# Performance work log

Measured on AMD Instinct MI355X. Metric: run time of the kernel, lower is better.

## Reference

```python
import jax, jax.numpy as jnp
import numpy as np

T, B = 32, 64
H, W = 16, 16
FEAT = 32
CNN_DIM = 512
N_ACT = 5
MAP_OUT = FEAT * H * W  # 8192, flattened map readout


def _conv_relu(x, w, b, stride):
    y = jax.lax.conv_general_dilated(
        x, w, (stride, stride), 'VALID',
        dimension_numbers=('NCHW', 'OIHW', 'NCHW'))
    return jax.nn.relu(y + b[None, :, None, None])


def _mlp(x, w1, b1, w2, b2):
    return jax.nn.relu(x @ w1 + b1) @ w2 + b2


def setup_inputs() -> dict:
    key = jax.random.key(0)
    ks = jax.random.split(key, 32)
    g = lambda k, shape, fan: jax.random.normal(k, shape, jnp.float32) * (1.0 / np.sqrt(fan))
    inp = {}
    inp['image'] = jax.random.uniform(ks[0], (T * B, 84, 84, 3), jnp.float32) * 255.0
    inp['done'] = jnp.zeros((T, B), jnp.float32)
    inp['state0'] = jnp.zeros((B, FEAT, H, W), jnp.float32)
    inp['position'] = jax.random.randint(ks[1], (T * B, 2), 0, H).astype(jnp.int32)
    # NatureCNN params
    inp['w1'] = g(ks[2], (32, 3, 8, 8), 3 * 8 * 8); inp['b1'] = jnp.zeros((32,), jnp.float32)
    inp['w2'] = g(ks[3], (64, 32, 4, 4), 32 * 4 * 4); inp['b2'] = jnp.zeros((64,), jnp.float32)
    inp['w3'] = g(ks[4], (64, 64, 3, 3), 64 * 3 * 3); inp['b3'] = jnp.zeros((64,), jnp.float32)
    inp['wfc'] = g(ks[5], (64 * 7 * 7, CNN_DIM), 64 * 7 * 7); inp['bfc'] = jnp.zeros((CNN_DIM,), jnp.float32)
    # Map write projection
    inp['Ww'] = g(ks[6], (CNN_DIM, FEAT), CNN_DIM); inp['bw'] = jnp.zeros((FEAT,), jnp.float32)
    # pos_net MLP: one-hot(16)+one-hot(16)=32 -> 64
    inp['wp1'] = g(ks[7], (2 * H, 64), 2 * H); inp['bp1'] = jnp.zeros((64,), jnp.float32)
    inp['wp2'] = g(ks[8], (64, 64), 64); inp['bp2'] = jnp.zeros((64,), jnp.float32)
    # policy MLP: (MAP_OUT+64) -> 64 -> N_ACT
    inp['wpo1'] = g(ks[9], (MAP_OUT + 64, 64), MAP_OUT + 64); inp['bpo1'] = jnp.zeros((64,), jnp.float32)
    inp['wpo2'] = g(ks[10], (64, N_ACT), 64) * 0.01; inp['bpo2'] = jnp.zeros((N_ACT,), jnp.float32)
    # value MLP
    inp['wv1'] = g(ks[11], (MAP_OUT + 64, 64), MAP_OUT + 64); inp['bv1'] = jnp.zeros((64,), jnp.float32)
    inp['wv2'] = g(ks[12], (64, 1), 64); inp['bv2'] = jnp.zeros((1,), jnp.float32)
    return inp


def reference(image, done, state0, w1, b1, w2, b2, w3, b3, wfc, bfc, Ww, bw,
              wp1, bp1, wp2, bp2, wpo1, bpo1, wpo2, bpo2, wv1, bv1, wv2, bv2,
              position):
    # preprocess_image: /255 and NHWC -> NCHW
    x = jnp.transpose(image / 255.0, (0, 3, 1, 2))
    x = _conv_relu(x, w1, b1, 4)   # [TB,32,20,20]
    x = _conv_relu(x, w2, b2, 2)   # [TB,64,9,9]
    x = _conv_relu(x, w3, b3, 1)   # [TB,64,7,7]
    h = jax.nn.relu(x.reshape(x.shape[0], -1) @ wfc + bfc)  # [TB,512]

    h_seq = h.reshape(T, B, CNN_DIM)
    idx_seq = position.reshape(T, B, 2)
    benv = jnp.arange(B)

    def step(state, inp):
        h_t, d_t, i_t = inp
        masked = (1.0 - d_t)[:, None, None, None] * state  # reset done envs
        wfeat = h_t @ Ww + bw                              # [B,FEAT]
        state = masked.at[benv, :, i_t[:, 0], i_t[:, 1]].add(wfeat)
        return state, state.reshape(B, -1)                 # per-step map readout

    state, outs = jax.lax.scan(step, state0, (h_seq, done, idx_seq))
    hidden = outs.reshape(T * B, MAP_OUT)

    # position net on one-hot coords
    pos_oh = jnp.concatenate([jax.nn.one_hot(position[:, 0], H, dtype=hidden.dtype),
                              jax.nn.one_hot(position[:, 1], W, dtype=hidden.dtype)], axis=1)
    pos_feat = _mlp(pos_oh, wp1, bp1, wp2, bp2)            # [TB,64]
    hidden = jnp.concatenate([hidden, pos_feat], axis=1)

    logits = _mlp(hidden, wpo1, bpo1, wpo2, bpo2)          # [TB,N_ACT]
    v = _mlp(hidden, wv1, bv1, wv2, bv2)                   # [TB,1]
    return logits, v, state
```

## Files before the change

### kernel.cpp

```cpp
#include <hip/hip_runtime.h>
#include <hip/hip_bf16.h>


#define TT 32
#define BB 64
#define TBR 2048

typedef _Float16 half_t;
typedef __attribute__((ext_vector_type(4))) _Float16 half4;
typedef __attribute__((ext_vector_type(8))) _Float16 half8;
typedef __attribute__((ext_vector_type(4))) float f32x4;

#define OFF_W1T   0u
#define OFF_W2T   6144u
#define OFF_W3T   22528u
#define OFF_WF    40960u
#define OFF_PF    106496u
#define OFF_Y0    237568u
#define OFF_YS    245760u
#define OFF_H     507904u
#define OFF_WFCT  1556480u
#define OFF_C3    2359296u
#define OFF_C2    5570560u
#define OFF_C1    10878976u

__global__ __launch_bounds__(256) void prep_kernel(
    const float* __restrict__ w1, const float* __restrict__ w2,
    const float* __restrict__ w3, half_t* __restrict__ w1p,
    half_t* __restrict__ w2T, half_t* __restrict__ w3T) {
  int g = blockIdx.x * 256 + threadIdx.x;
  if (g < 8192) {
    int kk = g & 31, oc = (g >> 5) & 31, tap = g >> 10;
    half_t v = (half_t)0.f;
    if (kk < 24) {
      int kx = kk / 3, c = kk - 3 * kx;
      v = (half_t)(w1[oc * 192 + c * 64 + tap * 8 + kx] * (1.0f / 255.0f));
    }
    w1p[g] = v;
    return;
  }
  int g2 = g - 8192;
  if (g2 < 32768) {
    int c = g2 & 31, oc = (g2 >> 5) & 63, tap = g2 >> 11;
    w2T[g2] = (half_t)w2[oc * 512 + c * 16 + tap];
    return;
  }
  int g3 = g2 - 32768;
  if (g3 < 36864) {
    int c = g3 & 63, oc = (g3 >> 6) & 63, tap = g3 >> 12;
    w3T[g3] = (half_t)w3[oc * 576 + c * 9 + tap];
  }
}

__global__ __launch_bounds__(256) void prep_wfct(
    const float* __restrict__ wfc, half_t* __restrict__ wfcT) {
  __shared__ float t[32][33];
  int k0 = blockIdx.x * 32, n0 = blockIdx.y * 32;
  int tx = threadIdx.x & 31, ty = threadIdx.x >> 5;
#pragma unroll
  for (int i = 0; i < 4; ++i)
    t[ty + 8 * i][tx] = wfc[(size_t)(k0 + ty + 8 * i) * 512 + n0 + tx];
  __syncthreads();
#pragma unroll
  for (int i = 0; i < 4; ++i)
    wfcT[(size_t)(n0 + ty + 8 * i) * 3136 + k0 + tx] =
        (half_t)t[tx][ty + 8 * i];
}

#define C1_BANDF 5040
#define C1_BANDV 1260
__global__ __launch_bounds__(256) void conv1_mfma(
    const float* __restrict__ img, const half_t* __restrict__ w1p,
    const float* __restrict__ b1, half_t* __restrict__ out, int n0) {
  __shared__ __align__(16) half_t As[2][C1_BANDF];
  int tid = threadIdx.x;
  int li = blockIdx.x;
  int w = tid >> 6, l = tid & 63, lc = l & 15, q = l >> 4;
  const float* ib = img + (size_t)(n0 + li) * 21168;
  half_t* ob = out + (size_t)li * 400 * 32;

  half8 bfrag[8][2];
#pragma unroll
  for (int tap = 0; tap < 8; ++tap)
#pragma unroll
    for (int t = 0; t < 2; ++t)
      bfrag[tap][t] =
          *(const half8*)(w1p + (size_t)(tap * 32 + t * 16 + lc) * 32 + q * 8);
  float b1v[2] = {b1[lc], b1[16 + lc]};

  f32x4 fr[5];
#define C1_LOADB(b)                                                   \
  {                                                                   \
    const float* src = ib + 4032 * (b);                               \
    _Pragma("unroll") for (int i = 0; i < 5; ++i) {                   \
      int g = tid + 256 * i;                                          \
      if (g < C1_BANDV) fr[i] = *(const f32x4*)(src + 4 * g);         \
    }                                                                 \
  }
#define C1_WRITEB(buf)                                                \
  {                                                                   \
    _Pragma("unroll") for (int i = 0; i < 5; ++i) {                   \
      int g = tid + 256 * i;                                          \
      if (g < C1_BANDV) {                                             \
        half4 o;                                                      \
        _Pragma("unroll") for (int j = 0; j < 4; ++j)                 \
            o[j] = (half_t)fr[i][j];                                  \
        *(half4*)&As[buf][4 * g] = o;                                 \
      }                                                               \
    }                                                                 \
  }

  C1_LOADB(0);
  C1_WRITEB(0);
  for (int b = 0; b < 5; ++b) {
    if (b < 4) C1_LOADB(b + 1);
    __syncthreads();
    int buf = b & 1;
    for (int tile = w; tile < 5; tile += 4) {
      int lp = tile * 16 + lc;
      int oyl = lp / 20, ox = lp - oyl * 20;
      f32x4 acc[2];
      acc[0] = (f32x4){0.f, 0.f, 0.f, 0.f};
      acc[1] = (f32x4){0.f, 0.f, 0.f, 0.f};
#pragma unroll
      for (int ky = 0; ky < 8; ++ky) {
        half8 af;
        if (q < 3) {
          const half_t* p = &As[buf][(4 * oyl + ky) * 252 + 12 * ox + q * 8];
          *(half4*)&af = *(const half4*)p;
          *((half4*)&af + 1) = *((const half4*)(p + 4));
        } else {
#pragma unroll
          for (int j = 0; j < 8; ++j) af[j] = (half_t)0.f;
        }
        acc[0] = __builtin_amdgcn_mfma_f32_16x16x32_f16(af, bfrag[ky][0],
                                                        acc[0], 0, 0, 0);
        acc[1] = __builtin_amdgcn_mfma_f32_16x16x32_f16(af, bfrag[ky][1],
                                                        acc[1], 0, 0, 0);
      }
#pragma unroll
      for (int t = 0; t < 2; ++t) {
#pragma unroll
        for (int r = 0; r < 4; ++r) {
          int mr = b * 80 + tile * 16 + q * 4 + r;
          ob[(size_t)mr * 32 + t * 16 + lc] =
              (half_t)fmaxf(acc[t][r] + b1v[t], 0.f);
        }
      }
    }
    if (b < 4) C1_WRITEB((b + 1) & 1);
  }
}

__global__ __launch_bounds__(256) void conv2_mfma(
    const half_t* __restrict__ in, const half_t* __restrict__ w2T,
    const float* __restrict__ b2, half_t* __restrict__ out, int n0) {
  __shared__ __align__(16) half_t As[12800];
  int tid = threadIdx.x;
  int li = blockIdx.x;
  int w = tid >> 6, l = tid & 63, lc = l & 15, q = l >> 4;
  const half_t* inb = in + (size_t)li * 12800;

#pragma unroll
  for (int i = 0; i < 7; ++i) {
    int ci = tid + 256 * i;
    if (ci < 1600) {
      uint4 v = *(const uint4*)(inb + ci * 8);
      int ip = ci >> 2, sp = ip >> 1;
      int u = ((ip & 1) << 6) | ((ci & 3) << 4);
      int byte = sp * 128 + (u ^ ((sp & 7) << 4));
      *(uint4*)((char*)As + byte) = v;
    }
  }

  half8 bfrag[16][2];
#pragma unroll
  for (int tap = 0; tap < 16; ++tap)
#pragma unroll
    for (int j = 0; j < 2; ++j) {
      int nt = (w & 1) * 2 + j;
      bfrag[tap][j] =
          *(const half8*)(w2T + (size_t)(tap * 64 + nt * 16 + lc) * 32 + q * 8);
    }
  float b2v[2];
#pragma unroll
  for (int j = 0; j < 2; ++j) b2v[j] = b2[(w & 1) * 32 + j * 16 + lc];

  __syncthreads();

  half_t* ob = out + (size_t)(n0 + li) * 5184;
#pragma unroll
  for (int ti = 0; ti < 3; ++ti) {
    int tile = (w >> 1) + 2 * ti;
    int row16 = tile * 16 + lc;
    int orow = row16 < 81 ? row16 : 80;
    int oy = orow / 9, ox = orow - oy * 9;
    f32x4 acc[2];
    acc[0] = (f32x4){0.f, 0.f, 0.f, 0.f};
    acc[1] = (f32x4){0.f, 0.f, 0.f, 0.f};
#pragma unroll
    for (int tap = 0; tap < 16; ++tap) {
      int ky = tap >> 2, kx = tap & 3;
      int ip = (2 * oy + ky) * 20 + 2 * ox + kx;
      int sp = ip >> 1;
      int u = ((ip & 1) << 6) | (q << 4);
      int byte = sp * 128 + (u ^ ((sp & 7) << 4));
      half8 af = *(const half8*)((const char*)As + byte);
      acc[0] = __builtin_amdgcn_mfma_f32_16x16x32_f16(af, bfrag[tap][0],
                                                      acc[0], 0, 0, 0);
      acc[1] = __builtin_amdgcn_mfma_f32_16x16x32_f16(af, bfrag[tap][1],
                                                      acc[1], 0, 0, 0);
    }
#pragma unroll
    for (int j = 0; j < 2; ++j) {
#pragma unroll
      for (int r = 0; r < 4; ++r) {
        int mr = tile * 16 + q * 4 + r;
        if (mr < 81) {
          int col = (w & 1) * 32 + j * 16 + lc;
          ob[(size_t)mr * 64 + col] = (half_t)fmaxf(acc[j][r] + b2v[j], 0.f);
        }
      }
    }
  }
}

__global__ __launch_bounds__(256) void conv3_mfma(
    const half_t* __restrict__ in, const half_t* __restrict__ w3T,
    const float* __restrict__ b3, half_t* __restrict__ out) {
  __shared__ __align__(16) half_t As[5184];
  int tid = threadIdx.x;
  int li = blockIdx.x;
  int w = tid >> 6, l = tid & 63, lc = l & 15, q = l >> 4;
  const half_t* inb = in + (size_t)li * 5184;

#pragma unroll
  for (int i = 0; i < 3; ++i) {
    int ci = tid + 256 * i;
    if (ci < 648) {
      uint4 v = *(const uint4*)(inb + ci * 8);
      int ir = ci >> 3, cc = ci & 7;
      int byte = ir * 128 + (((cc << 4)) ^ ((ir & 7) << 4));
      *(uint4*)((char*)As + byte) = v;
    }
  }

  half8 bfrag[9][2];
#pragma unroll
  for (int tap = 0; tap < 9; ++tap)
#pragma unroll
    for (int ch = 0; ch < 2; ++ch)
      bfrag[tap][ch] = *(const half8*)(
          w3T + (size_t)(tap * 64 + w * 16 + lc) * 64 + ch * 32 + q * 8);
  float b3v = b3[w * 16 + lc];

  __syncthreads();

  half_t* ob = out + (size_t)li * 3136;
#pragma unroll
  for (int tile = 0; tile < 4; ++tile) {
    int row16 = tile * 16 + lc;
    int orow = row16 < 49 ? row16 : 48;
    int oy = orow / 7, ox = orow - oy * 7;
    f32x4 acc = (f32x4){0.f, 0.f, 0.f, 0.f};
#pragma unroll
    for (int tap = 0; tap < 9; ++tap) {
      int ky = tap / 3, kx = tap - ky * 3;
      int ir = (oy + ky) * 9 + ox + kx;
#pragma unroll
      for (int ch = 0; ch < 2; ++ch) {
        int byte = ir * 128 + (((ch << 6) | (q << 4)) ^ ((ir & 7) << 4));
        half8 af = *(const half8*)((const char*)As + byte);
        acc = __builtin_amdgcn_mfma_f32_16x16x32_f16(af, bfrag[tap][ch],
                                                     acc, 0, 0, 0);
      }
    }
#pragma unroll
    for (int r = 0; r < 4; ++r) {
      int pos = tile * 16 + q * 4 + r;
      if (pos < 49) {
        int col = w * 16 + lc;
        ob[(size_t)col * 49 + pos] = (half_t)fmaxf(acc[r] + b3v, 0.f);
      }
    }
  }
}

__global__ __launch_bounds__(256) void fc_mfma(
    const half_t* __restrict__ A, const half_t* __restrict__ Bt,
    const float* __restrict__ bias, float* __restrict__ C) {
  __shared__ __align__(16) half_t As[64 * 40];
  __shared__ __align__(16) half_t Bs[64 * 40];
  int tid = threadIdx.x;
  int m0 = blockIdx.y * 64, n0 = blockIdx.x * 64;
  int w = tid >> 6;
  int l = tid & 63;
  int lc = l & 15, q = l >> 4;
  int srow = tid >> 2, sseg = tid & 3;

  const half_t* aPtr = A + (size_t)(m0 + srow) * 3136 + sseg * 8;
  const half_t* bPtr = Bt + (size_t)(n0 + srow) * 3136 + sseg * 8;
  uint4 aReg = *(const uint4*)aPtr;
  uint4 bReg = *(const uint4*)bPtr;

  f32x4 acc[4];
#pragma unroll
  for (int t = 0; t < 4; ++t) acc[t] = (f32x4){0.f, 0.f, 0.f, 0.f};

  for (int k0 = 0; k0 < 3136; k0 += 32) {
    __syncthreads();
    *(uint4*)&As[srow * 40 + sseg * 8] = aReg;
    *(uint4*)&Bs[srow * 40 + sseg * 8] = bReg;
    __syncthreads();
    if (k0 + 32 < 3136) {
      aReg = *(const uint4*)(aPtr + k0 + 32);
      bReg = *(const uint4*)(bPtr + k0 + 32);
    }
    half8 af = *(const half8*)&As[(w * 16 + lc) * 40 + q * 8];
#pragma unroll
    for (int t = 0; t < 4; ++t) {
      half8 bf = *(const half8*)&Bs[(t * 16 + lc) * 40 + q * 8];
      acc[t] = __builtin_amdgcn_mfma_f32_16x16x32_f16(af, bf, acc[t], 0, 0, 0);
    }
  }
#pragma unroll
  for (int t = 0; t < 4; ++t) {
#pragma unroll
    for (int r = 0; r < 4; ++r) {
      int row = m0 + w * 16 + q * 4 + r;
      int col = n0 + t * 16 + lc;
      C[(size_t)row * 512 + col] = fmaxf(acc[t][r] + bias[col], 0.f);
    }
  }
}

__global__ __launch_bounds__(256) void wfeat_kernel(
    const float* __restrict__ h, const float* __restrict__ Ww,
    const float* __restrict__ bw, float* __restrict__ wf) {
  int g = blockIdx.x * 256 + threadIdx.x;
  int row = g >> 5, oc = g & 31;
  float acc = bw[oc];
  const float* hr = h + (size_t)row * 512;
#pragma unroll 8
  for (int k = 0; k < 512; ++k) acc += hr[k] * Ww[k * 32 + oc];
  wf[g] = acc;
}

__global__ __launch_bounds__(256) void posfeat_kernel(
    const int* __restrict__ pos, const float* __restrict__ wp1,
    const float* __restrict__ bp1, const float* __restrict__ wp2,
    const float* __restrict__ bp2, float* __restrict__ pf) {
  int row = (blockIdx.x * 256 + threadIdx.x) >> 6;
  int l = threadIdx.x & 63;
  int p0 = pos[row * 2], p1 = pos[row * 2 + 1];
  float t1 = fmaxf(wp1[p0 * 64 + l] + wp1[(16 + p1) * 64 + l] + bp1[l], 0.f);
  float acc = bp2[l];
#pragma unroll
  for (int k = 0; k < 64; ++k) acc += __shfl(t1, k) * wp2[k * 64 + l];
  pf[row * 64 + l] = acc;
}

__global__ __launch_bounds__(256) void y0_kernel(
    const float* __restrict__ s0, const float* __restrict__ wpo1,
    const float* __restrict__ wv1, float* __restrict__ y0) {
  __shared__ float red[128];
  int b = blockIdx.x >> 5, kc = blockIdx.x & 31;
  int n = threadIdx.x & 127, kh = threadIdx.x >> 7;
  const float* W = (n < 64) ? (wpo1 + n) : (wv1 + (n - 64));
  int k0 = kc * 256 + kh * 128;
  const float* s = s0 + (size_t)b * 8192 + k0;
  float acc = 0.f;
#pragma unroll 8
  for (int j = 0; j < 128; ++j) acc += s[j] * W[(size_t)(k0 + j) * 64];
  if (kh) red[n] = acc;
  __syncthreads();
  if (!kh) atomicAdd(y0 + b * 128 + n, acc + red[n]);
}

__global__ __launch_bounds__(128) void ystate_kernel(
    const float* __restrict__ y0, const float* __restrict__ done,
    const int* __restrict__ pos, const float* __restrict__ wf,
    const float* __restrict__ wpo1, const float* __restrict__ wv1,
    float* __restrict__ ys) {
  int b = blockIdx.x;
  int n = threadIdx.x;
  const float* W = (n < 64) ? (wpo1 + n) : (wv1 + (n - 64));
  float y = y0[b * 128 + n];
  for (int t = 0; t < TT; ++t) {
    int row = t * BB + b;
    float mask = 1.f - done[row];
    int off = pos[row * 2] * 16 + pos[row * 2 + 1];
    y *= mask;
    const float* wfr = wf + row * 32;
#pragma unroll
    for (int c = 0; c < 32; ++c) y += wfr[c] * W[(size_t)(c * 256 + off) * 64];
    ys[(size_t)row * 128 + n] = y;
  }
}

__global__ __launch_bounds__(256) void state_kernel(
    const float* __restrict__ s0, const float* __restrict__ done,
    const int* __restrict__ pos, const float* __restrict__ wf,
    float* __restrict__ out_state) {
  int b = blockIdx.x, tid = threadIdx.x;
  float s[32];
#pragma unroll
  for (int c = 0; c < 32; ++c) s[c] = s0[(size_t)b * 8192 + c * 256 + tid];
  for (int t = 0; t < TT; ++t) {
    int row = t * BB + b;
    float mask = 1.f - done[row];
    int off = pos[row * 2] * 16 + pos[row * 2 + 1];
#pragma unroll
    for (int c = 0; c < 32; ++c) s[c] *= mask;
    if (tid == off) {
#pragma unroll
      for (int c = 0; c < 32; ++c) s[c] += wf[row * 32 + c];
    }
  }
#pragma unroll
  for (int c = 0; c < 32; ++c) out_state[(size_t)b * 8192 + c * 256 + tid] = s[c];
}

__global__ __launch_bounds__(256) void head_kernel(
    const float* __restrict__ ys, const float* __restrict__ pf,
    const float* __restrict__ wpo1, const float* __restrict__ wv1,
    const float* __restrict__ bpo1, const float* __restrict__ bv1,
    const float* __restrict__ wpo2, const float* __restrict__ bpo2,
    const float* __restrict__ wv2, const float* __restrict__ bv2,
    float* __restrict__ logits, float* __restrict__ vout) {
  int row = (blockIdx.x * 256 + threadIdx.x) >> 6;
  int l = threadIdx.x & 63;
  float pfv = pf[row * 64 + l];
  float accp = bpo1[l] + ys[(size_t)row * 128 + l];
  float accv = bv1[l] + ys[(size_t)row * 128 + 64 + l];
#pragma unroll
  for (int k = 0; k < 64; ++k) {
    float pk = __shfl(pfv, k);
    accp += pk * wpo1[(size_t)(8192 + k) * 64 + l];
    accv += pk * wv1[(size_t)(8192 + k) * 64 + l];
  }
  float rp = fmaxf(accp, 0.f), rv = fmaxf(accv, 0.f);
#pragma unroll
  for (int a = 0; a < 5; ++a) {
    float pa = rp * wpo2[l * 5 + a];
#pragma unroll
    for (int m = 32; m >= 1; m >>= 1) pa += __shfl_xor(pa, m);
    if (l == 0) logits[row * 5 + a] = pa + bpo2[a];
  }
  float pv = rv * wv2[l];
#pragma unroll
  for (int m = 32; m >= 1; m >>= 1) pv += __shfl_xor(pv, m);
  if (l == 0) vout[row] = pv + bv2[0];
}

extern "C" void kernel_launch(void* const* d_in, const int* in_sizes, int n_in,
                              void* d_out, int out_size, void* d_ws, size_t ws_size,
                              hipStream_t stream) {
  const float* image = (const float*)d_in[0];
  const float* done = (const float*)d_in[1];
  const float* state0 = (const float*)d_in[2];
  const int* position = (const int*)d_in[3];
  const float* w1 = (const float*)d_in[4];
  const float* b1 = (const float*)d_in[5];
  const float* w2 = (const float*)d_in[6];
  const float* b2 = (const float*)d_in[7];
  const float* w3 = (const float*)d_in[8];
  const float* b3 = (const float*)d_in[9];
  const float* wfc = (const float*)d_in[10];
  const float* bfc = (const float*)d_in[11];
  const float* Ww = (const float*)d_in[12];
  const float* bw = (const float*)d_in[13];
  const float* wp1 = (const float*)d_in[14];
  const float* bp1 = (const float*)d_in[15];
  const float* wp2 = (const float*)d_in[16];
  const float* bp2 = (const float*)d_in[17];
  const float* wpo1 = (const float*)d_in[18];
  const float* bpo1 = (const float*)d_in[19];
  const float* wpo2 = (const float*)d_in[20];
  const float* bpo2 = (const float*)d_in[21];
  const float* wv1 = (const float*)d_in[22];
  const float* bv1 = (const float*)d_in[23];
  const float* wv2 = (const float*)d_in[24];
  const float* bv2 = (const float*)d_in[25];

  float* ws = (float*)d_ws;
  half_t* w1p = (half_t*)(ws + OFF_W1T);
  half_t* w2T = (half_t*)(ws + OFF_W2T);
  half_t* w3T = (half_t*)(ws + OFF_W3T);
  float* wf = ws + OFF_WF;
  float* pfb = ws + OFF_PF;
  float* y0 = ws + OFF_Y0;
  float* ysb = ws + OFF_YS;
  float* h = ws + OFF_H;
  half_t* wfcT = (half_t*)(ws + OFF_WFCT);
  half_t* c3b = (half_t*)(ws + OFF_C3);
  half_t* c2b = (half_t*)(ws + OFF_C2);
  half_t* c1b = (half_t*)(ws + OFF_C1);

  float* out = (float*)d_out;
  float* out_logits = out;
  float* out_v = out + 10240;
  float* out_state = out + 12288;

  int CS;
  if (ws_size >= (size_t)23986176 * 4) CS = 2048;
  else if (ws_size >= (size_t)17432576 * 4) CS = 1024;
  else CS = 512;
  int nc = TBR / CS;

  hipMemsetAsync(y0, 0, 8192 * sizeof(float), stream);
  prep_kernel<<<304, 256, 0, stream>>>(w1, w2, w3, w1p, w2T, w3T);
  prep_wfct<<<dim3(98, 16), 256, 0, stream>>>(wfc, wfcT);

  for (int c = 0; c < nc; ++c) {
    int n0 = c * CS;
    conv1_mfma<<<CS, 256, 0, stream>>>(image, w1p, b1, c1b, n0);
    conv2_mfma<<<CS, 256, 0, stream>>>(c1b, w2T, b2, c2b, n0);
  }
  conv3_mfma<<<TBR, 256, 0, stream>>>(c2b, w3T, b3, c3b);
  fc_mfma<<<dim3(8, 32), 256, 0, stream>>>(c3b, wfcT, bfc, h);
  wfeat_kernel<<<256, 256, 0, stream>>>(h, Ww, bw, wf);
  posfeat_kernel<<<512, 256, 0, stream>>>(position, wp1, bp1, wp2, bp2, pfb);
  y0_kernel<<<2048, 256, 0, stream>>>(state0, wpo1, wv1, y0);
  ystate_kernel<<<64, 128, 0, stream>>>(y0, done, position, wf, wpo1, wv1, ysb);
  state_kernel<<<64, 256, 0, stream>>>(state0, done, position, wf, out_state);
  head_kernel<<<512, 256, 0, stream>>>(ysb, pfb, wpo1, wv1, bpo1, bv1,
                                       wpo2, bpo2, wv2, bv2, out_logits, out_v);
}
```

Before: 520.0 us.

## Merge small kernels and split serial ystate into parallel delta plus scan

Merges the weight-prep kernels into one launch, and merges the wfeat, posfeat and y0 kernels into another. The serial per-env ystate loop previously did 32 gathers from wpo1/wv1 at every time step. Those gathers now run as a fully parallel delta computation across all 2048 rows, fused with the state kernel, and a light scan kernel applies the mask-and-add recurrence. This cuts launch count and shortens the sequential critical path, at the cost of a new workspace buffer and one more pass over memory.

Result: faster. 452.8 us (-12.9%).

```diff
diff --git a/kernel.cpp b/kernel.cpp
--- a/kernel.cpp
+++ b/kernel.cpp
@@ -19,43 +19,46 @@
 #define OFF_Y0    237568u
 #define OFF_YS    245760u
 #define OFF_H     507904u
-#define OFF_WFCT  1556480u
-#define OFF_C3    2359296u
-#define OFF_C2    5570560u
-#define OFF_C1    10878976u
-
-__global__ __launch_bounds__(256) void prep_kernel(
+#define OFF_DELTA 1556480u
+#define OFF_WFCT  1818624u
+#define OFF_C3    2621440u
+#define OFF_C2    5832704u
+#define OFF_C1    11141120u
+
+__global__ __launch_bounds__(256) void prep_all(
     const float* __restrict__ w1, const float* __restrict__ w2,
     const float* __restrict__ w3, half_t* __restrict__ w1p,
-    half_t* __restrict__ w2T, half_t* __restrict__ w3T) {
-  int g = blockIdx.x * 256 + threadIdx.x;
-  if (g < 8192) {
-    int kk = g & 31, oc = (g >> 5) & 31, tap = g >> 10;
-    half_t v = (half_t)0.f;
-    if (kk < 24) {
-      int kx = kk / 3, c = kk - 3 * kx;
-      v = (half_t)(w1[oc * 192 + c * 64 + tap * 8 + kx] * (1.0f / 255.0f));
-    }
-    w1p[g] = v;
-    return;
-  }
-  int g2 = g - 8192;
-  if (g2 < 32768) {
-    int c = g2 & 31, oc = (g2 >> 5) & 63, tap = g2 >> 11;
-    w2T[g2] = (half_t)w2[oc * 512 + c * 16 + tap];
-    return;
-  }
-  int g3 = g2 - 32768;
-  if (g3 < 36864) {
-    int c = g3 & 63, oc = (g3 >> 6) & 63, tap = g3 >> 12;
-    w3T[g3] = (half_t)w3[oc * 576 + c * 9 + tap];
-  }
-}
-
-__global__ __launch_bounds__(256) void prep_wfct(
+    half_t* __restrict__ w2T, half_t* __restrict__ w3T,
     const float* __restrict__ wfc, half_t* __restrict__ wfcT) {
   __shared__ float t[32][33];
-  int k0 = blockIdx.x * 32, n0 = blockIdx.y * 32;
+  int bx = blockIdx.x;
+  if (bx < 304) {
+    int g = bx * 256 + threadIdx.x;
+    if (g < 8192) {
+      int kk = g & 31, oc = (g >> 5) & 31, tap = g >> 10;
+      half_t v = (half_t)0.f;
+      if (kk < 24) {
+        int kx = kk / 3, c = kk - 3 * kx;
+        v = (half_t)(w1[oc * 192 + c * 64 + tap * 8 + kx] * (1.0f / 255.0f));
+      }
+      w1p[g] = v;
+      return;
+    }
+    int g2 = g - 8192;
+    if (g2 < 32768) {
+      int c = g2 & 31, oc = (g2 >> 5) & 63, tap = g2 >> 11;
+      w2T[g2] = (half_t)w2[oc * 512 + c * 16 + tap];
+      return;
+    }
+    int g3 = g2 - 32768;
+    if (g3 < 36864) {
+      int c = g3 & 63, oc = (g3 >> 6) & 63, tap = g3 >> 12;
+      w3T[g3] = (half_t)w3[oc * 576 + c * 9 + tap];
+    }
+    return;
+  }
+  int gb = bx - 304;
+  int k0 = (gb % 98) * 32, n0 = (gb / 98) * 32;
   int tx = threadIdx.x & 31, ty = threadIdx.x >> 5;
 #pragma unroll
   for (int i = 0; i < 4; ++i)
@@ -334,37 +337,39 @@
   }
 }
 
-__global__ __launch_bounds__(256) void wfeat_kernel(
+__global__ __launch_bounds__(256) void mid1_kernel(
     const float* __restrict__ h, const float* __restrict__ Ww,
-    const float* __restrict__ bw, float* __restrict__ wf) {
-  int g = blockIdx.x * 256 + threadIdx.x;
-  int row = g >> 5, oc = g & 31;
-  float acc = bw[oc];
-  const float* hr = h + (size_t)row * 512;
-#pragma unroll 8
-  for (int k = 0; k < 512; ++k) acc += hr[k] * Ww[k * 32 + oc];
-  wf[g] = acc;
-}
-
-__global__ __launch_bounds__(256) void posfeat_kernel(
+    const float* __restrict__ bw, float* __restrict__ wf,
     const int* __restrict__ pos, const float* __restrict__ wp1,
     const float* __restrict__ bp1, const float* __restrict__ wp2,
-    const float* __restrict__ bp2, float* __restrict__ pf) {
-  int row = (blockIdx.x * 256 + threadIdx.x) >> 6;
-  int l = threadIdx.x & 63;
-  int p0 = pos[row * 2], p1 = pos[row * 2 + 1];
-  float t1 = fmaxf(wp1[p0 * 64 + l] + wp1[(16 + p1) * 64 + l] + bp1[l], 0.f);
-  float acc = bp2[l];
-#pragma unroll
-  for (int k = 0; k < 64; ++k) acc += __shfl(t1, k) * wp2[k * 64 + l];
-  pf[row * 64 + l] = acc;
-}
-
-__global__ __launch_bounds__(256) void y0_kernel(
+    const float* __restrict__ bp2, float* __restrict__ pf,
     const float* __restrict__ s0, const float* __restrict__ wpo1,
     const float* __restrict__ wv1, float* __restrict__ y0) {
   __shared__ float red[128];
-  int b = blockIdx.x >> 5, kc = blockIdx.x & 31;
+  int bx = blockIdx.x;
+  if (bx < 256) {
+    int g = bx * 256 + threadIdx.x;
+    int row = g >> 5, oc = g & 31;
+    float acc = bw[oc];
+    const float* hr = h + (size_t)row * 512;
+#pragma unroll 8
+    for (int k = 0; k < 512; ++k) acc += hr[k] * Ww[k * 32 + oc];
+    wf[g] = acc;
+    return;
+  }
+  if (bx < 768) {
+    int row = ((bx - 256) * 256 + threadIdx.x) >> 6;
+    int l = threadIdx.x & 63;
+    int p0 = pos[row * 2], p1 = pos[row * 2 + 1];
+    float t1 = fmaxf(wp1[p0 * 64 + l] + wp1[(16 + p1) * 64 + l] + bp1[l], 0.f);
+    float acc = bp2[l];
+#pragma unroll
+    for (int k = 0; k < 64; ++k) acc += __shfl(t1, k) * wp2[k * 64 + l];
+    pf[row * 64 + l] = acc;
+    return;
+  }
+  int g = bx - 768;
+  int b = g >> 5, kc = g & 31;
   int n = threadIdx.x & 127, kh = threadIdx.x >> 7;
   const float* W = (n < 64) ? (wpo1 + n) : (wv1 + (n - 64));
   int k0 = kc * 256 + kh * 128;
@@ -377,32 +382,25 @@
   if (!kh) atomicAdd(y0 + b * 128 + n, acc + red[n]);
 }
 
-__global__ __launch_bounds__(128) void ystate_kernel(
-    const float* __restrict__ y0, const float* __restrict__ done,
+__global__ __launch_bounds__(256) void mid2_kernel(
     const int* __restrict__ pos, const float* __restrict__ wf,
     const float* __restrict__ wpo1, const float* __restrict__ wv1,
-    float* __restrict__ ys) {
-  int b = blockIdx.x;
-  int n = threadIdx.x;
-  const float* W = (n < 64) ? (wpo1 + n) : (wv1 + (n - 64));
-  float y = y0[b * 128 + n];
-  for (int t = 0; t < TT; ++t) {
-    int row = t * BB + b;
-    float mask = 1.f - done[row];
+    float* __restrict__ delta, const float* __restrict__ s0,
+    const float* __restrict__ done, float* __restrict__ out_state) {
+  int bx = blockIdx.x;
+  if (bx < 1024) {
+    int row = bx * 2 + (threadIdx.x >> 7);
+    int n = threadIdx.x & 127;
+    const float* W = (n < 64) ? (wpo1 + n) : (wv1 + (n - 64));
     int off = pos[row * 2] * 16 + pos[row * 2 + 1];
-    y *= mask;
     const float* wfr = wf + row * 32;
-#pragma unroll
-    for (int c = 0; c < 32; ++c) y += wfr[c] * W[(size_t)(c * 256 + off) * 64];
-    ys[(size_t)row * 128 + n] = y;
-  }
-}
-
-__global__ __launch_bounds__(256) void state_kernel(
-    const float* __restrict__ s0, const float* __restrict__ done,
-    const int* __restrict__ pos, const float* __restrict__ wf,
-    float* __restrict__ out_state) {
-  int b = blockIdx.x, tid = threadIdx.x;
+    float d = 0.f;
+#pragma unroll
+    for (int c = 0; c < 32; ++c) d += wfr[c] * W[(size_t)(c * 256 + off) * 64];
+    delta[(size_t)row * 128 + n] = d;
+    return;
+  }
+  int b = bx - 1024, tid = threadIdx.x;
   float s[32];
 #pragma unroll
   for (int c = 0; c < 32; ++c) s[c] = s0[(size_t)b * 8192 + c * 256 + tid];
@@ -419,6 +417,19 @@
   }
 #pragma unroll
   for (int c = 0; c < 32; ++c) out_state[(size_t)b * 8192 + c * 256 + tid] = s[c];
+}
+
+__global__ __launch_bounds__(128) void scan_kernel(
+    const float* __restrict__ y0, const float* __restrict__ done,
+    const float* __restrict__ delta, float* __restrict__ ys) {
+  int b = blockIdx.x;
+  int n = threadIdx.x;
+  float y = y0[b * 128 + n];
+  for (int t = 0; t < TT; ++t) {
+    int row = t * BB + b;
+    y = y * (1.f - done[row]) + delta[(size_t)row * 128 + n];
+    ys[(size_t)row * 128 + n] = y;
+  }
 }
 
 __global__ __launch_bounds__(256) void head_kernel(
@@ -492,6 +503,7 @@
   float* y0 = ws + OFF_Y0;
   float* ysb = ws + OFF_YS;
   float* h = ws + OFF_H;
+  float* deltab = ws + OFF_DELTA;
   half_t* wfcT = (half_t*)(ws + OFF_WFCT);
   half_t* c3b = (half_t*)(ws + OFF_C3);
   half_t* c2b = (half_t*)(ws + OFF_C2);
@@ -503,14 +515,13 @@
   float* out_state = out + 12288;
 
   int CS;
-  if (ws_size >= (size_t)23986176 * 4) CS = 2048;
-  else if (ws_size >= (size_t)17432576 * 4) CS = 1024;
+  if (ws_size >= (size_t)24248320 * 4) CS = 2048;
+  else if (ws_size >= (size_t)17694720 * 4) CS = 1024;
   else CS = 512;
   int nc = TBR / CS;
 
   hipMemsetAsync(y0, 0, 8192 * sizeof(float), stream);
-  prep_kernel<<<304, 256, 0, stream>>>(w1, w2, w3, w1p, w2T, w3T);
-  prep_wfct<<<dim3(98, 16), 256, 0, stream>>>(wfc, wfcT);
+  prep_all<<<1872, 256, 0, stream>>>(w1, w2, w3, w1p, w2T, w3T, wfc, wfcT);
 
   for (int c = 0; c < nc; ++c) {
     int n0 = c * CS;
@@ -519,11 +530,11 @@
   }
   conv3_mfma<<<TBR, 256, 0, stream>>>(c2b, w3T, b3, c3b);
   fc_mfma<<<dim3(8, 32), 256, 0, stream>>>(c3b, wfcT, bfc, h);
-  wfeat_kernel<<<256, 256, 0, stream>>>(h, Ww, bw, wf);
-  posfeat_kernel<<<512, 256, 0, stream>>>(position, wp1, bp1, wp2, bp2, pfb);
-  y0_kernel<<<2048, 256, 0, stream>>>(state0, wpo1, wv1, y0);
-  ystate_kernel<<<64, 128, 0, stream>>>(y0, done, position, wf, wpo1, wv1, ysb);
-  state_kernel<<<64, 256, 0, stream>>>(state0, done, position, wf, out_state);
+  mid1_kernel<<<2816, 256, 0, stream>>>(h, Ww, bw, wf, position, wp1, bp1,
+                                        wp2, bp2, pfb, state0, wpo1, wv1, y0);
+  mid2_kernel<<<1088, 256, 0, stream>>>(position, wf, wpo1, wv1, deltab,
+                                        state0, done, out_state);
+  scan_kernel<<<64, 128, 0, stream>>>(y0, done, deltab, ysb);
   head_kernel<<<512, 256, 0, stream>>>(ysb, pfb, wpo1, wv1, bpo1, bv1,
                                        wpo2, bpo2, wv2, bv2, out_logits, out_v);
 }
```
